# Kernel tuning notes

Hardware: AMD Instinct MI355X
Metric: run time of the kernel (lower is better)

## Reference

```python
import jax, jax.numpy as jnp
import numpy as np

D = 64          # slot_size == in_features
S = 8           # num_slots
H = 128         # mlp_hidden_size
N_ITER = 3
EPS = 1e-8


def _ln(x, g, b, eps=1e-5):
    m = jnp.mean(x, axis=-1, keepdims=True)
    v = jnp.var(x, axis=-1, keepdims=True)
    return (x - m) * jax.lax.rsqrt(v + eps) * g + b


def _gru(x, h, w_ih, w_hh, b_ih, b_hh):
    # torch.nn.GRUCell semantics, gate order r, z, n
    gi = x @ w_ih.T + b_ih
    gh = h @ w_hh.T + b_hh
    i_r, i_z, i_n = jnp.split(gi, 3, axis=-1)
    h_r, h_z, h_n = jnp.split(gh, 3, axis=-1)
    r = jax.nn.sigmoid(i_r + h_r)
    z = jax.nn.sigmoid(i_z + h_z)
    n = jnp.tanh(i_n + r * h_n)
    return (1.0 - z) * n + z * h


def setup_inputs() -> dict:
    key = jax.random.key(0)
    ks = jax.random.split(key, 16)
    sc = 0.02
    inp = {
        'inputs': jax.random.normal(ks[0], (64, 16384, D), jnp.float32),
        'slots_init': jax.random.normal(ks[1], (64, S, D), jnp.float32),
        'ln_in_g': jnp.ones((D,), jnp.float32), 'ln_in_b': jnp.zeros((D,), jnp.float32),
        'ln_s_g': jnp.ones((D,), jnp.float32), 'ln_s_b': jnp.zeros((D,), jnp.float32),
        'ln_m_g': jnp.ones((D,), jnp.float32), 'ln_m_b': jnp.zeros((D,), jnp.float32),
        'Wq': jax.random.normal(ks[2], (D, D), jnp.float32) * sc,
        'Wk': jax.random.normal(ks[3], (D, D), jnp.float32) * sc,
        'Wv': jax.random.normal(ks[4], (D, D), jnp.float32) * sc,
        'w_ih': jax.random.normal(ks[5], (3 * D, D), jnp.float32) * sc,
        'w_hh': jax.random.normal(ks[6], (3 * D, D), jnp.float32) * sc,
        'b_ih': jnp.zeros((3 * D,), jnp.float32),
        'b_hh': jnp.zeros((3 * D,), jnp.float32),
        'W1': jax.random.normal(ks[7], (H, D), jnp.float32) * sc,
        'b1': jnp.zeros((H,), jnp.float32),
        'W2': jax.random.normal(ks[8], (D, H), jnp.float32) * sc,
        'b2': jnp.zeros((D,), jnp.float32),
        'slots_mu': jax.random.normal(ks[9], (1, 1, D), jnp.float32) * sc,
        'slots_log_sigma': jax.random.normal(ks[10], (1, 1, D), jnp.float32) * sc,
    }
    return inp


def reference(inputs, slots_init, ln_in_g, ln_in_b, ln_s_g, ln_s_b, ln_m_g, ln_m_b,
              Wq, Wk, Wv, w_ih, w_hh, b_ih, b_hh, W1, b1, W2, b2,
              slots_mu, slots_log_sigma):
    B, N, _ = inputs.shape
    x = _ln(inputs, ln_in_g, ln_in_b)
    k = x @ Wk.T                               # [B, N, D]
    v = x @ Wv.T                               # [B, N, D]
    slots = slots_mu + jnp.exp(slots_log_sigma) * slots_init  # [B, S, D]
    scale = D ** -0.5
    attns = None
    for it in range(N_ITER):
        slots_prev = slots
        sn = _ln(slots, ln_s_g, ln_s_b)
        q = sn @ Wq.T                          # [B, S, D]
        logits = scale * jnp.einsum('bnd,bsd->bns', k, q)  # [B, N, S]
        attn = jax.nn.softmax(logits, axis=-1)
        if it == 0:
            attns = jax.lax.stop_gradient(attn)  # clone().detach() on first iter
        else:
            attns = attns + attn
        a = attn + EPS
        a = a / jnp.sum(a, axis=1, keepdims=True)  # normalize over inputs
        updates = jnp.einsum('bns,bnd->bsd', a, v)  # [B, S, D]
        h = _gru(updates.reshape(B * S, D), slots_prev.reshape(B * S, D),
                 w_ih, w_hh, b_ih, b_hh).reshape(B, S, D)
        mlp_out = jnp.maximum(_ln(h, ln_m_g, ln_m_b) @ W1.T + b1, 0.0) @ W2.T + b2
        slots = h + mlp_out
    return slots, attns / N_ITER
```

## Files before the change

kernel.cpp:

```cpp
#include <hip/hip_runtime.h>
#include <math.h>

#define Dk 64
#define Sk 8
#define Nk 16384
#define Bk 64
#define Hk 128
#define BSD (Bk*Sk*Dk)

typedef __attribute__((ext_vector_type(8))) short   bf16x8;
typedef __attribute__((ext_vector_type(4))) float   f32x4;
typedef __attribute__((ext_vector_type(2))) unsigned int u32x2;
typedef __attribute__((ext_vector_type(4))) unsigned int u32x4;

union FragU { u32x4 u; bf16x8 s; };

__device__ __forceinline__ unsigned short f2b(float f){
  unsigned u = __float_as_uint(f);
  unsigned r = (u + 0x7FFFu + ((u>>16)&1u)) >> 16;
  return (unsigned short)r;
}
__device__ __forceinline__ unsigned pk2(float a, float b){
  return (unsigned)f2b(a) | ((unsigned)f2b(b)<<16);
}
__device__ __forceinline__ bf16x8 mkfrag(unsigned a0,unsigned a1,unsigned a2,unsigned a3){
  FragU x; x.u = (u32x4){a0,a1,a2,a3}; return x.s;
}
__device__ __forceinline__ bf16x8 mkfrag2(u32x2 a, u32x2 b){
  FragU x; x.u = (u32x4){a.x,a.y,b.x,b.y}; return x.s;
}
__device__ __forceinline__ float wsum64(float v){
  #pragma unroll
  for (int m=1;m<64;m<<=1) v += __shfl_xor(v,m,64);
  return v;
}
__device__ __forceinline__ f32x4 ntld4(const float* p){
  return __builtin_nontemporal_load((const f32x4*)p);
}

#define MFMA16(a,b,c) __builtin_amdgcn_mfma_f32_16x16x32_bf16(a,b,c,0,0,0)
#define TRRD(dst, addr)          asm volatile("ds_read_b64_tr_b16 %0, %1"              : "=v"(dst) : "v"(addr) : "memory")
#define TRRD_O(dst, addr, OFF)   asm volatile("ds_read_b64_tr_b16 %0, %1 offset:" #OFF : "=v"(dst) : "v"(addr) : "memory")

template<int MODE, int LAST>
__global__ __launch_bounds__(256,4) void iter_kernel(
    const float* __restrict__ inp, unsigned short* __restrict__ xbf,
    const float* __restrict__ ln_g, const float* __restrict__ ln_b,
    const float* __restrict__ qtb,
    float* __restrict__ attns_out,
    float* __restrict__ Upart,
    float* __restrict__ denpart)
{
  constexpr int NQ = LAST ? 3 : 1;
  __shared__ unsigned short shmem[4*2688];
  __shared__ float ured[4][512];
  __shared__ float dred[4][8];

  const int t   = threadIdx.x;
  const int wid = t>>6, l = t&63;
  const int r16 = l&15, g = l>>4;
  unsigned short* sh = &shmem[wid*2688];
  const unsigned ldsb = (unsigned)(unsigned long long)(void*)sh;

  const int blk = blockIdx.x;
  const int gw  = blk*4 + wid;
  const int b   = gw>>7;
  const int w0  = (gw&127)*4;

  bf16x8 qf0[NQ], qf1[NQ];
  #pragma unroll
  for (int it=0; it<NQ; ++it){
    const float* qp = qtb + (size_t)it*BSD + (size_t)((b<<3) + (r16&7))*Dk + g*8;
    f32x4 a0 = *(const f32x4*)(qp);    f32x4 a1 = *(const f32x4*)(qp+4);
    f32x4 c0 = *(const f32x4*)(qp+32); f32x4 c1 = *(const f32x4*)(qp+36);
    qf0[it] = mkfrag(pk2(a0.x,a0.y),pk2(a0.z,a0.w),pk2(a1.x,a1.y),pk2(a1.z,a1.w));
    qf1[it] = mkfrag(pk2(c0.x,c0.y),pk2(c0.z,c0.w),pk2(c1.x,c1.y),pk2(c1.z,c1.w));
  }

  f32x4 uacc0={0.f,0.f,0.f,0.f}, uacc1={0.f,0.f,0.f,0.f};
  f32x4 uacc2={0.f,0.f,0.f,0.f}, uacc3={0.f,0.f,0.f,0.f};
  f32x4 dacc = {0.f,0.f,0.f,0.f};

  f32x4 gv0,gv1,gv2,gv3, bv0,bv1,bv2,bv3;
  if (MODE==0){
    const float* gp = ln_g + g*16; const float* bp = ln_b + g*16;
    gv0=*(const f32x4*)gp;     gv1=*(const f32x4*)(gp+4);
    gv2=*(const f32x4*)(gp+8); gv3=*(const f32x4*)(gp+12);
    bv0=*(const f32x4*)bp;     bv1=*(const f32x4*)(bp+4);
    bv2=*(const f32x4*)(bp+8); bv3=*(const f32x4*)(bp+12);
  }

  f32x4 cx[2][4];
  u32x4 cp[2][2];
  {
    const size_t rw0 = (size_t)b*Nk + (size_t)w0*32;
    if (MODE==0){
      #pragma unroll
      for (int rt=0; rt<2; ++rt){
        const float* src = inp + (rw0 + rt*16 + r16)*Dk + g*16;
        cx[rt][0]=ntld4(src);   cx[rt][1]=ntld4(src+4);
        cx[rt][2]=ntld4(src+8); cx[rt][3]=ntld4(src+12);
      }
    } else {
      #pragma unroll
      for (int rt=0; rt<2; ++rt){
        const unsigned short* sp = xbf + (rw0 + rt*16 + r16)*Dk;
        cp[rt][0] = *(const u32x4*)(sp + g*8);
        cp[rt][1] = *(const u32x4*)(sp + 32 + g*8);
      }
    }
  }

  for (int w4=0; w4<4; ++w4){
    const size_t rowwin = (size_t)b*Nk + (size_t)(w0+w4)*32;
    bf16x8 xf00, xf01, xf10, xf11;

    if (MODE==0){
      #pragma unroll
      for (int rt=0; rt<2; ++rt){
        const int rloc = rt*16 + r16;
        const size_t row = rowwin + rloc;
        f32x4 x0=cx[rt][0], x1=cx[rt][1], x2=cx[rt][2], x3=cx[rt][3];
        float s1 = (x0.x+x0.y+x0.z+x0.w)+(x1.x+x1.y+x1.z+x1.w)
                 + (x2.x+x2.y+x2.z+x2.w)+(x3.x+x3.y+x3.z+x3.w);
        float s2 = x0.x*x0.x+x0.y*x0.y+x0.z*x0.z+x0.w*x0.w
                 + x1.x*x1.x+x1.y*x1.y+x1.z*x1.z+x1.w*x1.w
                 + x2.x*x2.x+x2.y*x2.y+x2.z*x2.z+x2.w*x2.w
                 + x3.x*x3.x+x3.y*x3.y+x3.z*x3.z+x3.w*x3.w;
        s1 += __shfl_xor(s1,16,64); s1 += __shfl_xor(s1,32,64);
        s2 += __shfl_xor(s2,16,64); s2 += __shfl_xor(s2,32,64);
        const float mean = s1*(1.f/64.f);
        const float rstd = rsqrtf(s2*(1.f/64.f) - mean*mean + 1e-5f);
        x0 = (x0-mean)*rstd*gv0 + bv0;  x1 = (x1-mean)*rstd*gv1 + bv1;
        x2 = (x2-mean)*rstd*gv2 + bv2;  x3 = (x3-mean)*rstd*gv3 + bv3;
        u32x4 lo = {pk2(x0.x,x0.y),pk2(x0.z,x0.w),pk2(x1.x,x1.y),pk2(x1.z,x1.w)};
        u32x4 hi = {pk2(x2.x,x2.y),pk2(x2.z,x2.w),pk2(x3.x,x3.y),pk2(x3.z,x3.w)};
        u32x4* dst = (u32x4*)(xbf + row*Dk + g*16);
        dst[0] = lo; dst[1] = hi;
        const int sb = g*528 + rloc*16;
        *(u32x4*)&sh[sb]   = lo;
        *(u32x4*)&sh[sb+8] = hi;
      }
    } else {
      #pragma unroll
      for (int rt=0; rt<2; ++rt){
        const int rloc = rt*16 + r16;
        FragU f0, f1; f0.u = cp[rt][0]; f1.u = cp[rt][1];
        if (rt==0){ xf00=f0.s; xf01=f1.s; } else { xf10=f0.s; xf11=f1.s; }
        const int i0 = (g>>1)*528     + rloc*16 + (g&1)*8;
        const int i1 = ((g>>1)+2)*528 + rloc*16 + (g&1)*8;
        *(u32x4*)&sh[i0] = cp[rt][0];
        *(u32x4*)&sh[i1] = cp[rt][1];
      }
    }

    if (w4 < 3){
      const size_t rwn = rowwin + 32;
      if (MODE==0){
        #pragma unroll
        for (int rt=0; rt<2; ++rt){
          const float* src = inp + (rwn + rt*16 + r16)*Dk + g*16;
          cx[rt][0]=ntld4(src);   cx[rt][1]=ntld4(src+4);
          cx[rt][2]=ntld4(src+8); cx[rt][3]=ntld4(src+12);
        }
      } else {
        #pragma unroll
        for (int rt=0; rt<2; ++rt){
          const unsigned short* sp = xbf + (rwn + rt*16 + r16)*Dk;
          cp[rt][0] = *(const u32x4*)(sp + g*8);
          cp[rt][1] = *(const u32x4*)(sp + 32 + g*8);
        }
      }
    }

    if (MODE==0){
      #pragma unroll
      for (int rt=0; rt<2; ++rt){
        const int rloc = rt*16 + r16;
        const int i0 = (g>>1)*528     + rloc*16 + (g&1)*8;
        const int i1 = ((g>>1)+2)*528 + rloc*16 + (g&1)*8;
        FragU f0, f1;
        f0.u = *(const u32x4*)&sh[i0];
        f1.u = *(const u32x4*)&sh[i1];
        if (rt==0){ xf00=f0.s; xf01=f1.s; } else { xf10=f0.s; xf11=f1.s; }
      }
    }

    #pragma unroll
    for (int rt=0; rt<2; ++rt){
      const bf16x8 xl = rt ? xf10 : xf00;
      const bf16x8 xh = rt ? xf11 : xf01;
      f32x4 asum = {0.f,0.f,0.f,0.f};
      f32x4 atc;
      #pragma unroll
      for (int it=0; it<NQ; ++it){
        f32x4 c = {0.f,0.f,0.f,0.f};
        c = MFMA16(qf0[it], xl, c);
        c = MFMA16(qf1[it], xh, c);
        float mx = fmaxf(fmaxf(c.x,c.y), fmaxf(c.z,c.w));
        mx = fmaxf(mx, __shfl_xor(mx,16,64));
        f32x4 e;
        e.x = __expf(c.x-mx); e.y = __expf(c.y-mx);
        e.z = __expf(c.z-mx); e.w = __expf(c.w-mx);
        float es = e.x+e.y+e.z+e.w;
        es += __shfl_xor(es,16,64);
        f32x4 at = e*(1.f/es);
        if (LAST) asum = asum + at;
        atc = at;
      }
      if (LAST && l < 32){
        f32x4 nv = asum*(1.f/3.f);
        __builtin_nontemporal_store(nv,
            (f32x4*)(attns_out + (rowwin + rt*16 + r16)*Sk + g*4));
      }
      f32x4 a = atc + 1e-8f;
      dacc = dacc + a;
      u32x2 pk = {pk2(a.x,a.y), pk2(a.z,a.w)};
      *(u32x2*)&sh[2112 + (rt*16+r16)*16 + g*4] = pk;
    }

    asm volatile("s_waitcnt lgkmcnt(0)" ::: "memory");
    u32x2 p0,p1, b00,b01,b10,b11,b20,b21,b30,b31;
    const unsigned pA = ldsb + 4224 + g*256 + r16*2;
    TRRD  (p0, pA);
    TRRD_O(p1, pA, 128);
    const unsigned xA = ldsb + g*256 + r16*2;
    TRRD  (b00, xA);          TRRD_O(b01, xA, 128);
    TRRD_O(b10, xA, 1056);    TRRD_O(b11, xA, 1184);
    TRRD_O(b20, xA, 2112);    TRRD_O(b21, xA, 2240);
    TRRD_O(b30, xA, 3168);    TRRD_O(b31, xA, 3296);
    asm volatile("s_waitcnt lgkmcnt(0)" ::: "memory");
    __builtin_amdgcn_sched_barrier(0);
    const bf16x8 pf = mkfrag2(p0,p1);
    uacc0 = MFMA16(pf, mkfrag2(b00,b01), uacc0);
    uacc1 = MFMA16(pf, mkfrag2(b10,b11), uacc1);
    uacc2 = MFMA16(pf, mkfrag2(b20,b21), uacc2);
    uacc3 = MFMA16(pf, mkfrag2(b30,b31), uacc3);
  }

  float dd0=dacc.x, dd1=dacc.y, dd2=dacc.z, dd3=dacc.w;
  #pragma unroll
  for (int m=1;m<16;m<<=1){
    dd0 += __shfl_xor(dd0,m,64); dd1 += __shfl_xor(dd1,m,64);
    dd2 += __shfl_xor(dd2,m,64); dd3 += __shfl_xor(dd3,m,64);
  }
  if (l < 32){
    #pragma unroll
    for (int j=0;j<4;++j){
      ured[wid][(g*4+j)*64 +  0 + r16] = uacc0[j];
      ured[wid][(g*4+j)*64 + 16 + r16] = uacc1[j];
      ured[wid][(g*4+j)*64 + 32 + r16] = uacc2[j];
      ured[wid][(g*4+j)*64 + 48 + r16] = uacc3[j];
    }
    if (r16 == 0){
      dred[wid][g*4+0]=dd0; dred[wid][g*4+1]=dd1;
      dred[wid][g*4+2]=dd2; dred[wid][g*4+3]=dd3;
    }
  }
  __syncthreads();
  #pragma unroll
  for (int e=t; e<512; e+=256){
    Upart[(size_t)blk*512 + e] = ured[0][e]+ured[1][e]+ured[2][e]+ured[3][e];
  }
  if (t < 8) denpart[blk*8 + t] = dred[0][t]+dred[1][t]+dred[2][t]+dred[3][t];
}

__global__ __launch_bounds__(64) void slot_kernel(
    const float* __restrict__ slots_init,
    const float* __restrict__ mu, const float* __restrict__ lsig,
    const float* __restrict__ ln_s_g, const float* __restrict__ ln_s_b,
    const float* __restrict__ ln_m_g, const float* __restrict__ ln_m_b,
    const float* __restrict__ Wq, const float* __restrict__ Wk, const float* __restrict__ Wv,
    const float* __restrict__ w_ih, const float* __restrict__ w_hh,
    const float* __restrict__ b_ih, const float* __restrict__ b_hh,
    const float* __restrict__ W1, const float* __restrict__ b1,
    const float* __restrict__ W2, const float* __restrict__ b2,
    float* __restrict__ slots, const float* __restrict__ Upart,
    const float* __restrict__ denpart,
    float* __restrict__ qt_out, float* __restrict__ slots_out, int mode)
{
  __shared__ float sh[Hk];
  __shared__ float shh[Dk];
  const int d  = threadIdx.x;
  const int bs = blockIdx.x;

  float snew;
  if (mode == 0) {
    snew = mu[d] + expf(lsig[d]) * slots_init[bs*Dk + d];
  } else {
    const int b8 = bs>>3, s = bs&7;
    const float* up = Upart + (size_t)(b8*32)*512 + s*64 + d;
    float uval = 0.f;
    #pragma unroll 8
    for (int k2=0;k2<32;++k2) uval += up[k2*512];
    float dp = (d<32) ? denpart[(b8*32+d)*8 + s] : 0.f;
    const float dn = wsum64(dp);

    sh[d] = uval;
    __syncthreads();
    float num = 0.f;
    #pragma unroll
    for (int j=0;j<Dk;j+=4){
      float4 w = *(const float4*)&Wv[d*Dk+j];
      num += sh[j]*w.x + sh[j+1]*w.y + sh[j+2]*w.z + sh[j+3]*w.w;
    }
    const float upd = num / dn;
    const float h = slots[bs*Dk + d];
    __syncthreads();
    sh[d] = upd; shh[d] = h;
    __syncthreads();

    float gi_r=b_ih[d], gi_z=b_ih[Dk+d], gi_n=b_ih[2*Dk+d];
    float gh_r=b_hh[d], gh_z=b_hh[Dk+d], gh_n=b_hh[2*Dk+d];
    #pragma unroll 4
    for (int j=0;j<Dk;j+=4){
      const float x0=sh[j],  x1=sh[j+1],  x2=sh[j+2],  x3=sh[j+3];
      const float h0=shh[j], h1=shh[j+1], h2=shh[j+2], h3=shh[j+3];
      float4 w;
      w = *(const float4*)&w_ih[d*Dk+j];        gi_r += x0*w.x+x1*w.y+x2*w.z+x3*w.w;
      w = *(const float4*)&w_ih[(Dk+d)*Dk+j];   gi_z += x0*w.x+x1*w.y+x2*w.z+x3*w.w;
      w = *(const float4*)&w_ih[(2*Dk+d)*Dk+j]; gi_n += x0*w.x+x1*w.y+x2*w.z+x3*w.w;
      w = *(const float4*)&w_hh[d*Dk+j];        gh_r += h0*w.x+h1*w.y+h2*w.z+h3*w.w;
      w = *(const float4*)&w_hh[(Dk+d)*Dk+j];   gh_z += h0*w.x+h1*w.y+h2*w.z+h3*w.w;
      w = *(const float4*)&w_hh[(2*Dk+d)*Dk+j]; gh_n += h0*w.x+h1*w.y+h2*w.z+h3*w.w;
    }
    const float rg = 1.f/(1.f+expf(-(gi_r+gh_r)));
    const float zg = 1.f/(1.f+expf(-(gi_z+gh_z)));
    const float ng = tanhf(gi_n + rg*gh_n);
    const float hn = (1.f-zg)*ng + zg*h;

    const float m  = wsum64(hn)*(1.f/64.f);
    const float dv = hn - m;
    const float vr = wsum64(dv*dv)*(1.f/64.f);
    const float mv = dv*rsqrtf(vr+1e-5f)*ln_m_g[d] + ln_m_b[d];
    __syncthreads();
    sh[d] = mv;
    __syncthreads();

    float h1a = b1[d], h2a = b1[Dk+d];
    #pragma unroll 4
    for (int j=0;j<Dk;j+=4){
      const float x0=sh[j], x1=sh[j+1], x2=sh[j+2], x3=sh[j+3];
      float4 w;
      w = *(const float4*)&W1[d*Dk+j];      h1a += x0*w.x+x1*w.y+x2*w.z+x3*w.w;
      w = *(const float4*)&W1[(Dk+d)*Dk+j]; h2a += x0*w.x+x1*w.y+x2*w.z+x3*w.w;
    }
    h1a = fmaxf(h1a, 0.f); h2a = fmaxf(h2a, 0.f);
    __syncthreads();
    sh[d] = h1a; sh[Dk+d] = h2a;
    __syncthreads();
    float o = b2[d];
    #pragma unroll 4
    for (int tt=0;tt<Hk;tt+=4){
      float4 w = *(const float4*)&W2[d*Hk+tt];
      o += sh[tt]*w.x + sh[tt+1]*w.y + sh[tt+2]*w.z + sh[tt+3]*w.w;
    }
    snew = hn + o;
  }

  slots[bs*Dk + d] = snew;
  if (slots_out) slots_out[bs*Dk + d] = snew;

  const float m2  = wsum64(snew)*(1.f/64.f);
  const float dv2 = snew - m2;
  const float vr2 = wsum64(dv2*dv2)*(1.f/64.f);
  const float sn  = dv2*rsqrtf(vr2+1e-5f)*ln_s_g[d] + ln_s_b[d];
  __syncthreads();
  sh[d] = sn;
  __syncthreads();
  float q = 0.f;
  #pragma unroll
  for (int j=0;j<Dk;j+=4){
    float4 w = *(const float4*)&Wq[d*Dk+j];
    q += sh[j]*w.x + sh[j+1]*w.y + sh[j+2]*w.z + sh[j+3]*w.w;
  }
  __syncthreads();
  sh[d] = q;
  __syncthreads();
  float qt = 0.f;
  for (int dd=0; dd<Dk; ++dd) qt += sh[dd]*Wk[dd*Dk + d];
  qt_out[bs*Dk + d] = qt * 0.125f;
}

extern "C" void kernel_launch(void* const* d_in, const int* in_sizes, int n_in,
                              void* d_out, int out_size, void* d_ws, size_t ws_size,
                              hipStream_t stream)
{
  const float* inp     = (const float*)d_in[0];
  const float* sinit   = (const float*)d_in[1];
  const float* ln_in_g = (const float*)d_in[2];
  const float* ln_in_b = (const float*)d_in[3];
  const float* ln_s_g  = (const float*)d_in[4];
  const float* ln_s_b  = (const float*)d_in[5];
  const float* ln_m_g  = (const float*)d_in[6];
  const float* ln_m_b  = (const float*)d_in[7];
  const float* Wq      = (const float*)d_in[8];
  const float* Wk      = (const float*)d_in[9];
  const float* Wv      = (const float*)d_in[10];
  const float* w_ih    = (const float*)d_in[11];
  const float* w_hh    = (const float*)d_in[12];
  const float* b_ih    = (const float*)d_in[13];
  const float* b_hh    = (const float*)d_in[14];
  const float* W1      = (const float*)d_in[15];
  const float* b1      = (const float*)d_in[16];
  const float* W2      = (const float*)d_in[17];
  const float* b2      = (const float*)d_in[18];
  const float* mu      = (const float*)d_in[19];
  const float* lsig    = (const float*)d_in[20];

  float* out       = (float*)d_out;
  float* out_slots = out;
  float* out_attns = out + BSD;

  char* w = (char*)d_ws;
  float* slots   = (float*)(w);
  float* qtbuf   = (float*)(w + 131072);
  float* Upart   = (float*)(w + 655360);
  float* denpart = (float*)(w + 4849664);
  unsigned short* xbf = (unsigned short*)(w + 4915200);

  float* qt0 = qtbuf;
  float* qt1 = qtbuf + BSD;
  float* qt2 = qtbuf + 2*BSD;
  float* qt3 = qtbuf + 3*BSD;

  slot_kernel<<<Bk*Sk, Dk, 0, stream>>>(sinit, mu, lsig, ln_s_g, ln_s_b, ln_m_g, ln_m_b,
      Wq, Wk, Wv, w_ih, w_hh, b_ih, b_hh, W1, b1, W2, b2,
      slots, Upart, denpart, qt0, nullptr, 0);

  iter_kernel<0,0><<<2048, 256, 0, stream>>>(
      inp, xbf, ln_in_g, ln_in_b, qt0, out_attns, Upart, denpart);
  slot_kernel<<<Bk*Sk, Dk, 0, stream>>>(sinit, mu, lsig, ln_s_g, ln_s_b, ln_m_g, ln_m_b,
      Wq, Wk, Wv, w_ih, w_hh, b_ih, b_hh, W1, b1, W2, b2,
      slots, Upart, denpart, qt1, nullptr, 1);

  iter_kernel<1,0><<<2048, 256, 0, stream>>>(
      inp, xbf, ln_in_g, ln_in_b, qt1, out_attns, Upart, denpart);
  slot_kernel<<<Bk*Sk, Dk, 0, stream>>>(sinit, mu, lsig, ln_s_g, ln_s_b, ln_m_g, ln_m_b,
      Wq, Wk, Wv, w_ih, w_hh, b_ih, b_hh, W1, b1, W2, b2,
      slots, Upart, denpart, qt2, nullptr, 1);

  iter_kernel<1,1><<<2048, 256, 0, stream>>>(
      inp, xbf, ln_in_g, ln_in_b, qtbuf, out_attns, Upart, denpart);
  slot_kernel<<<Bk*Sk, Dk, 0, stream>>>(sinit, mu, lsig, ln_s_g, ln_s_b, ln_m_g, ln_m_b,
      Wq, Wk, Wv, w_ih, w_hh, b_ih, b_hh, W1, b1, W2, b2,
      slots, Upart, denpart, qt3, out_slots, 1);
}
```

Measured before the change: 249.5 us.

## Software-pipeline window processing and drop LDS round-trip for input fragments

The input loop is restructured into LOADW/PROCESS stages. The next window's layernorm, bf16 packing and LDS stores are issued while the current window's transposed LDS reads are still in flight, and global prefetch now runs two windows ahead. The fp32 per-lane load layout changes to g*8 and 32+g*8, so MODE 0 can build MFMA fragments straight from registers instead of writing to LDS and reading back. A partial lgkmcnt wait replaces the full drains, which adds register pressure and relies on in-order LDS completion. The final slots kernel also returns early after writing the output, skipping the unused next-q computation.

Measured after the change: 232.1 us. 1.07x faster.

```diff
diff --git a/kernel.cpp b/kernel.cpp
--- a/kernel.cpp
+++ b/kernel.cpp
@@ -83,44 +83,44 @@
 
   f32x4 gv0,gv1,gv2,gv3, bv0,bv1,bv2,bv3;
   if (MODE==0){
-    const float* gp = ln_g + g*16; const float* bp = ln_b + g*16;
-    gv0=*(const f32x4*)gp;     gv1=*(const f32x4*)(gp+4);
-    gv2=*(const f32x4*)(gp+8); gv3=*(const f32x4*)(gp+12);
-    bv0=*(const f32x4*)bp;     bv1=*(const f32x4*)(bp+4);
-    bv2=*(const f32x4*)(bp+8); bv3=*(const f32x4*)(bp+12);
-  }
-
-  f32x4 cx[2][4];
-  u32x4 cp[2][2];
-  {
-    const size_t rw0 = (size_t)b*Nk + (size_t)w0*32;
-    if (MODE==0){
-      #pragma unroll
-      for (int rt=0; rt<2; ++rt){
-        const float* src = inp + (rw0 + rt*16 + r16)*Dk + g*16;
-        cx[rt][0]=ntld4(src);   cx[rt][1]=ntld4(src+4);
-        cx[rt][2]=ntld4(src+8); cx[rt][3]=ntld4(src+12);
+    const float* gp  = ln_g + g*8;      const float* bp  = ln_b + g*8;
+    const float* gp2 = ln_g + 32 + g*8; const float* bp2 = ln_b + 32 + g*8;
+    gv0=*(const f32x4*)gp;  gv1=*(const f32x4*)(gp+4);
+    gv2=*(const f32x4*)gp2; gv3=*(const f32x4*)(gp2+4);
+    bv0=*(const f32x4*)bp;  bv1=*(const f32x4*)(bp+4);
+    bv2=*(const f32x4*)bp2; bv3=*(const f32x4*)(bp2+4);
+  }
+
+  f32x4 nx[2][4];
+  u32x4 np[2][2];
+  u32x4 fr[2][2];
+
+  auto LOADW = [&](int w){
+    const size_t base = (size_t)b*Nk + (size_t)(w0+w)*32;
+    #pragma unroll
+    for (int rt=0; rt<2; ++rt){
+      const size_t row = base + rt*16 + r16;
+      if (MODE==0){
+        const float* s0 = inp + row*Dk + g*8;
+        const float* s1 = inp + row*Dk + 32 + g*8;
+        nx[rt][0]=ntld4(s0); nx[rt][1]=ntld4(s0+4);
+        nx[rt][2]=ntld4(s1); nx[rt][3]=ntld4(s1+4);
+      } else {
+        const unsigned short* sp = xbf + row*Dk;
+        np[rt][0] = *(const u32x4*)(sp + g*8);
+        np[rt][1] = *(const u32x4*)(sp + 32 + g*8);
       }
-    } else {
-      #pragma unroll
-      for (int rt=0; rt<2; ++rt){
-        const unsigned short* sp = xbf + (rw0 + rt*16 + r16)*Dk;
-        cp[rt][0] = *(const u32x4*)(sp + g*8);
-        cp[rt][1] = *(const u32x4*)(sp + 32 + g*8);
-      }
-    }
-  }
-
-  for (int w4=0; w4<4; ++w4){
-    const size_t rowwin = (size_t)b*Nk + (size_t)(w0+w4)*32;
-    bf16x8 xf00, xf01, xf10, xf11;
-
-    if (MODE==0){
-      #pragma unroll
-      for (int rt=0; rt<2; ++rt){
-        const int rloc = rt*16 + r16;
-        const size_t row = rowwin + rloc;
-        f32x4 x0=cx[rt][0], x1=cx[rt][1], x2=cx[rt][2], x3=cx[rt][3];
+    }
+  };
+
+  auto PROCESS = [&](int w){
+    const size_t base = (size_t)b*Nk + (size_t)(w0+w)*32;
+    #pragma unroll
+    for (int rt=0; rt<2; ++rt){
+      const int rloc = rt*16 + r16;
+      u32x4 q0, q1;
+      if (MODE==0){
+        f32x4 x0=nx[rt][0], x1=nx[rt][1], x2=nx[rt][2], x3=nx[rt][3];
         float s1 = (x0.x+x0.y+x0.z+x0.w)+(x1.x+x1.y+x1.z+x1.w)
                  + (x2.x+x2.y+x2.z+x2.w)+(x3.x+x3.y+x3.z+x3.w);
         float s2 = x0.x*x0.x+x0.y*x0.y+x0.z*x0.z+x0.w*x0.w
@@ -133,63 +133,31 @@
         const float rstd = rsqrtf(s2*(1.f/64.f) - mean*mean + 1e-5f);
         x0 = (x0-mean)*rstd*gv0 + bv0;  x1 = (x1-mean)*rstd*gv1 + bv1;
         x2 = (x2-mean)*rstd*gv2 + bv2;  x3 = (x3-mean)*rstd*gv3 + bv3;
-        u32x4 lo = {pk2(x0.x,x0.y),pk2(x0.z,x0.w),pk2(x1.x,x1.y),pk2(x1.z,x1.w)};
-        u32x4 hi = {pk2(x2.x,x2.y),pk2(x2.z,x2.w),pk2(x3.x,x3.y),pk2(x3.z,x3.w)};
-        u32x4* dst = (u32x4*)(xbf + row*Dk + g*16);
-        dst[0] = lo; dst[1] = hi;
-        const int sb = g*528 + rloc*16;
-        *(u32x4*)&sh[sb]   = lo;
-        *(u32x4*)&sh[sb+8] = hi;
+        q0 = (u32x4){pk2(x0.x,x0.y),pk2(x0.z,x0.w),pk2(x1.x,x1.y),pk2(x1.z,x1.w)};
+        q1 = (u32x4){pk2(x2.x,x2.y),pk2(x2.z,x2.w),pk2(x3.x,x3.y),pk2(x3.z,x3.w)};
+        const size_t row = base + rloc;
+        *(u32x4*)(xbf + row*Dk + g*8)      = q0;
+        *(u32x4*)(xbf + row*Dk + 32 + g*8) = q1;
+      } else {
+        q0 = np[rt][0]; q1 = np[rt][1];
       }
-    } else {
-      #pragma unroll
-      for (int rt=0; rt<2; ++rt){
-        const int rloc = rt*16 + r16;
-        FragU f0, f1; f0.u = cp[rt][0]; f1.u = cp[rt][1];
-        if (rt==0){ xf00=f0.s; xf01=f1.s; } else { xf10=f0.s; xf11=f1.s; }
-        const int i0 = (g>>1)*528     + rloc*16 + (g&1)*8;
-        const int i1 = ((g>>1)+2)*528 + rloc*16 + (g&1)*8;
-        *(u32x4*)&sh[i0] = cp[rt][0];
-        *(u32x4*)&sh[i1] = cp[rt][1];
-      }
-    }
-
-    if (w4 < 3){
-      const size_t rwn = rowwin + 32;
-      if (MODE==0){
-        #pragma unroll
-        for (int rt=0; rt<2; ++rt){
-          const float* src = inp + (rwn + rt*16 + r16)*Dk + g*16;
-          cx[rt][0]=ntld4(src);   cx[rt][1]=ntld4(src+4);
-          cx[rt][2]=ntld4(src+8); cx[rt][3]=ntld4(src+12);
-        }
-      } else {
-        #pragma unroll
-        for (int rt=0; rt<2; ++rt){
-          const unsigned short* sp = xbf + (rwn + rt*16 + r16)*Dk;
-          cp[rt][0] = *(const u32x4*)(sp + g*8);
-          cp[rt][1] = *(const u32x4*)(sp + 32 + g*8);
-        }
-      }
-    }
-
-    if (MODE==0){
-      #pragma unroll
-      for (int rt=0; rt<2; ++rt){
-        const int rloc = rt*16 + r16;
-        const int i0 = (g>>1)*528     + rloc*16 + (g&1)*8;
-        const int i1 = ((g>>1)+2)*528 + rloc*16 + (g&1)*8;
-        FragU f0, f1;
-        f0.u = *(const u32x4*)&sh[i0];
-        f1.u = *(const u32x4*)&sh[i1];
-        if (rt==0){ xf00=f0.s; xf01=f1.s; } else { xf10=f0.s; xf11=f1.s; }
-      }
-    }
+      fr[rt][0] = q0; fr[rt][1] = q1;
+      const int i0 = (g>>1)*528     + rloc*16 + (g&1)*8;
+      const int i1 = ((g>>1)+2)*528 + rloc*16 + (g&1)*8;
+      *(u32x4*)&sh[i0] = q0;
+      *(u32x4*)&sh[i1] = q1;
+    }
+  };
+
+  LOADW(0); PROCESS(0); LOADW(1);
+
+  for (int w4=0; w4<4; ++w4){
+    const size_t rowwin = (size_t)b*Nk + (size_t)(w0+w4)*32;
 
     #pragma unroll
     for (int rt=0; rt<2; ++rt){
-      const bf16x8 xl = rt ? xf10 : xf00;
-      const bf16x8 xh = rt ? xf11 : xf01;
+      FragU fl, fh; fl.u = fr[rt][0]; fh.u = fr[rt][1];
+      const bf16x8 xl = fl.s, xh = fh.s;
       f32x4 asum = {0.f,0.f,0.f,0.f};
       f32x4 atc;
       #pragma unroll
@@ -219,18 +187,22 @@
       *(u32x2*)&sh[2112 + (rt*16+r16)*16 + g*4] = pk;
     }
 
-    asm volatile("s_waitcnt lgkmcnt(0)" ::: "memory");
     u32x2 p0,p1, b00,b01,b10,b11,b20,b21,b30,b31;
+    const unsigned xA = ldsb + g*256 + r16*2;
     const unsigned pA = ldsb + 4224 + g*256 + r16*2;
-    TRRD  (p0, pA);
-    TRRD_O(p1, pA, 128);
-    const unsigned xA = ldsb + g*256 + r16*2;
     TRRD  (b00, xA);          TRRD_O(b01, xA, 128);
     TRRD_O(b10, xA, 1056);    TRRD_O(b11, xA, 1184);
     TRRD_O(b20, xA, 2112);    TRRD_O(b21, xA, 2240);
     TRRD_O(b30, xA, 3168);    TRRD_O(b31, xA, 3296);
-    asm volatile("s_waitcnt lgkmcnt(0)" ::: "memory");
+    TRRD  (p0, pA);           TRRD_O(p1, pA, 128);
+
+    if (w4 < 3) PROCESS(w4+1);
+    if (w4 < 2) LOADW(w4+2);
+
+    if (w4 < 3) asm volatile("s_waitcnt lgkmcnt(4)" ::: "memory");
+    else        asm volatile("s_waitcnt lgkmcnt(0)" ::: "memory");
     __builtin_amdgcn_sched_barrier(0);
+
     const bf16x8 pf = mkfrag2(p0,p1);
     uacc0 = MFMA16(pf, mkfrag2(b00,b01), uacc0);
     uacc1 = MFMA16(pf, mkfrag2(b10,b11), uacc1);
@@ -358,8 +330,8 @@
     snew = hn + o;
   }
 
+  if (slots_out){ slots_out[bs*Dk + d] = snew; return; }
   slots[bs*Dk + d] = snew;
-  if (slots_out) slots_out[bs*Dk + d] = snew;
 
   const float m2  = wsum64(snew)*(1.f/64.f);
   const float dv2 = snew - m2;
```
